# Kernel optimization log

Measured on AMD Instinct MI355X. Metric: run time of the kernel, lower is better.

Reference implementation:

```python
import jax, jax.numpy as jnp
import numpy as np

N, E, IN, H, C = 50000, 800000, 128, 256, 2
EPS = 1e-5


def setup_inputs() -> dict:
    key = jax.random.key(0)
    ks = jax.random.split(key, 12)
    inp = {
        "x": jax.random.normal(ks[0], (N, IN), jnp.float32),
        "edge_index": jax.random.randint(ks[1], (2, E), 0, N, jnp.int32),
        "w_nei0": jax.random.normal(ks[2], (IN, H), jnp.float32) * 0.05,
        "w_root0": jax.random.normal(ks[3], (IN, H), jnp.float32) * 0.05,
        "b0": jnp.zeros((H,), jnp.float32),
        "w_nei": jax.random.normal(ks[4], (2, H, H), jnp.float32) * 0.05,
        "w_root": jax.random.normal(ks[5], (2, H, H), jnp.float32) * 0.05,
        "b": jnp.zeros((2, H), jnp.float32),
        "bn_gamma": jnp.ones((3, H), jnp.float32),
        "bn_beta": jnp.zeros((3, H), jnp.float32),
        "bn_mean": jax.random.normal(ks[6], (3, H), jnp.float32) * 0.05,
        "bn_var": jnp.ones((3, H), jnp.float32),
        "w1": jax.random.normal(ks[7], (H, H // 2), jnp.float32) * 0.05,
        "b1": jnp.zeros((H // 2,), jnp.float32),
        "w2": jax.random.normal(ks[8], (H // 2, C), jnp.float32) * 0.05,
        "b2": jnp.zeros((C,), jnp.float32),
    }
    return inp


def _mean_aggregate(h, src, dst, inv_deg):
    # gather source-node features, scatter-sum to destinations, divide by degree
    agg = jax.ops.segment_sum(h[src], dst, num_segments=N)  # (N, d)
    return agg * inv_deg[:, None]


def _forward(x, edge_index, w_nei0, w_root0, b0, w_nei, w_root, b,
             bn_gamma, bn_beta, bn_mean, bn_var, w1, b1, w2, b2):
    src, dst = edge_index[0], edge_index[1]
    deg = jax.ops.segment_sum(jnp.ones((E,), x.dtype), dst, num_segments=N)
    inv_deg = 1.0 / jnp.maximum(deg, 1.0)

    h = x
    wn_list = [w_nei0, w_nei[0], w_nei[1]]
    wr_list = [w_root0, w_root[0], w_root[1]]
    bias_list = [b0, b[0], b[1]]
    for i in range(3):
        mean_nb = _mean_aggregate(h, src, dst, inv_deg)          # (N, d_in)
        h = mean_nb @ wn_list[i] + bias_list[i] + h @ wr_list[i]  # SAGEConv
        # BatchNorm1d (eval: running stats) + ReLU; dropout is identity in eval
        h = (h - bn_mean[i]) * jax.lax.rsqrt(bn_var[i] + EPS) * bn_gamma[i] + bn_beta[i]
        h = jax.nn.relu(h)

    h = jax.nn.relu(h @ w1 + b1)
    logits = h @ w2 + b2
    return jax.nn.log_softmax(logits, axis=1)


def reference(x, edge_index, w_nei0, w_root0, b0, w_nei, w_root, b,
              bn_gamma, bn_beta, bn_mean, bn_var, w1, b1, w2, b2):
    return _forward(x, edge_index, w_nei0, w_root0, b0, w_nei, w_root, b,
                    bn_gamma, bn_beta, bn_mean, bn_var, w1, b1, w2, b2)
```

## Files before the change

### kernel.cpp

```cpp
#include <hip/hip_runtime.h>
#include <hip/hip_fp16.h>

#define N_NODES 50000
#define N_EDGES 800000
#define DIM_IN 128
#define DIM_H 256

typedef _Float16 f16;
typedef _Float16 half8 __attribute__((ext_vector_type(8)));
typedef _Float16 f16x4 __attribute__((ext_vector_type(4)));
typedef _Float16 f16x2 __attribute__((ext_vector_type(2)));
typedef float f32x4 __attribute__((ext_vector_type(4)));
typedef unsigned int u32;

__device__ __forceinline__ void gload_lds16(const void* g, void* l) {
    __builtin_amdgcn_global_load_lds(
        (const __attribute__((address_space(1))) u32*)g,
        (__attribute__((address_space(3))) u32*)l,
        16, 0, 0);
}


__global__ void k_deg(const int* __restrict__ dst, int* __restrict__ deg) {
    int i = blockIdx.x * 256 + threadIdx.x;
    if (i < N_EDGES) atomicAdd(&deg[dst[i]], 1);
}

__global__ void k_scan1(const int* __restrict__ deg, int* __restrict__ row_start,
                        int* __restrict__ partials) {
    __shared__ int sm[256];
    int t = threadIdx.x;
    int i = blockIdx.x * 256 + t;
    int v = (i < N_NODES) ? deg[i] : 0;
    sm[t] = v;
    __syncthreads();
    for (int ofs = 1; ofs < 256; ofs <<= 1) {
        int add = (t >= ofs) ? sm[t - ofs] : 0;
        __syncthreads();
        sm[t] += add;
        __syncthreads();
    }
    if (i < N_NODES) row_start[i] = sm[t] - v;
    if (t == 255) partials[blockIdx.x] = sm[255];
}

__global__ void k_scan2(const int* __restrict__ partials, int* __restrict__ pscan, int nblk) {
    __shared__ int sm[256];
    int t = threadIdx.x;
    int v = (t < nblk) ? partials[t] : 0;
    sm[t] = v;
    __syncthreads();
    for (int ofs = 1; ofs < 256; ofs <<= 1) {
        int add = (t >= ofs) ? sm[t - ofs] : 0;
        __syncthreads();
        sm[t] += add;
        __syncthreads();
    }
    pscan[t] = sm[t] - v;
}

__global__ void k_scan3(const int* __restrict__ deg, int* __restrict__ row_start,
                        const int* __restrict__ pscan, float* __restrict__ inv_deg) {
    int i = blockIdx.x * 256 + threadIdx.x;
    if (i < N_NODES) {
        row_start[i] += pscan[blockIdx.x];
        int d = deg[i];
        inv_deg[i] = 1.0f / (float)(d > 1 ? d : 1);
        if (i == 0) row_start[N_NODES] = N_EDGES;
    }
}

__global__ void k_fill(const int* __restrict__ src, const int* __restrict__ dst,
                       const int* __restrict__ row_start, int* __restrict__ cursor,
                       int* __restrict__ csr) {
    int i = blockIdx.x * 256 + threadIdx.x;
    if (i < N_EDGES) {
        int d = dst[i];
        int p = atomicAdd(&cursor[d], 1);
        csr[row_start[d] + p] = src[i];
    }
}


__global__ void k_cvt_x(const float* __restrict__ x, f16* __restrict__ o) {
    int i = blockIdx.x * 256 + threadIdx.x;
    if (i < N_NODES * DIM_IN / 4) {
        float4 v = ((const float4*)x)[i];
        f16x4 h = {(f16)v.x, (f16)v.y, (f16)v.z, (f16)v.w};
        *(f16x4*)(o + (size_t)i * 4) = h;
    }
}

__global__ void k_tcvt(const float* __restrict__ W, f16* __restrict__ Wt, int K, int NN) {
    int t = blockIdx.x * 256 + threadIdx.x;
    if (t < K * NN) {
        int n = t / K, k = t - n * K;
        Wt[t] = (f16)W[(size_t)k * NN + n];
    }
}

__global__ void k_st(const float* __restrict__ b0, const float* __restrict__ bvec,
                     const float* __restrict__ gamma, const float* __restrict__ beta,
                     const float* __restrict__ mean, const float* __restrict__ var,
                     const float* __restrict__ b1, float* __restrict__ st) {
    int c = threadIdx.x;
    for (int layer = 0; layer < 3; layer++) {
        float bias = (layer == 0) ? b0[c] : bvec[(layer - 1) * DIM_H + c];
        float g = gamma[layer * DIM_H + c];
        float be = beta[layer * DIM_H + c];
        float mu = mean[layer * DIM_H + c];
        float va = var[layer * DIM_H + c];
        float s = g * rsqrtf(va + 1e-5f);
        st[layer * 512 + c] = s;
        st[layer * 512 + 256 + c] = (bias - mu) * s + be;
    }
    st[3 * 512 + c] = 1.0f;
    st[3 * 512 + 256 + c] = (c < 128) ? b1[c] : 0.0f;
}


template <int D>
__global__ void k_agg(const f16* __restrict__ h, const int* __restrict__ row_start,
                      const int* __restrict__ csr, const float* __restrict__ inv_deg,
                      f16* __restrict__ agg) {
    constexpr int V = D / 64;
    typedef _Float16 fvec __attribute__((ext_vector_type(V)));
    int wid = threadIdx.x >> 6;
    int lane = threadIdx.x & 63;
    int v = blockIdx.x * 4 + wid;
    if (v >= N_NODES) return;
    int e0 = row_start[v], e1 = row_start[v + 1];
    float acc[V];
#pragma unroll
    for (int j = 0; j < V; j++) acc[j] = 0.0f;

    const int li = lane & 15;
    for (int e = e0; e < e1; e += 16) {
        int ee = e + li;
        int idx = csr[ee < e1 ? ee : e1 - 1];
        int rem = e1 - e;
        fvec hv[16];
#pragma unroll
        for (int j = 0; j < 16; j++) {
            int s = __shfl(idx, j);
            hv[j] = *(const fvec*)(h + (size_t)s * D + lane * V);
        }
#pragma unroll
        for (int j = 0; j < 16; j++) {
            if (j < rem) {
#pragma unroll
                for (int q = 0; q < V; q++) acc[q] += (float)hv[j][q];
            }
        }
    }

    float sc = inv_deg[v];
    fvec o;
#pragma unroll
    for (int j = 0; j < V; j++) o[j] = (f16)(acc[j] * sc);
    *(fvec*)(agg + (size_t)v * D + lane * V) = o;
}


__global__ __launch_bounds__(256) void k_gemm(
    const f16* __restrict__ A1, int lda1, const f16* __restrict__ B1, int k1,
    const f16* __restrict__ A2, int lda2, const f16* __restrict__ B2, int k2,
    const float* __restrict__ sc, const float* __restrict__ sh,
    f16* __restrict__ out, int ldo, int M) {
    __shared__ f16 aT[2][64 * 32];
    __shared__ f16 bT[2][256 * 32];
    const int tid = threadIdx.x;
    const int lane = tid & 63;
    const int wid = tid >> 6;
    const int m0 = blockIdx.x * 64;
    f32x4 acc[4][4] = {};

    const int srow = tid >> 2;
    const int schunk = (tid & 3) ^ ((tid >> 3) & 3);
    const int ktot = k1 + k2;

    auto stage = [&](int buf, int kk) {
        const f16 *Ap, *Bp;
        int lda, ldb, kloc;
        if (kk < k1) { Ap = A1; Bp = B1; lda = lda1; ldb = k1; kloc = kk; }
        else         { Ap = A2; Bp = B2; lda = lda2; ldb = k2; kloc = kk - k1; }
        int gm = m0 + srow;
        gm = gm < M ? gm : M - 1;
        gload_lds16(Ap + (size_t)gm * lda + kloc + schunk * 8,
                    (char*)&aT[buf][0] + tid * 16);
#pragma unroll
        for (int hh = 0; hh < 4; hh++) {
            gload_lds16(Bp + (size_t)(hh * 64 + srow) * ldb + kloc + schunk * 8,
                        (char*)&bT[buf][0] + hh * 4096 + tid * 16);
        }
    };

    auto compute = [&](int buf) {
        half8 af[4], bf[4];
#pragma unroll
        for (int mi = 0; mi < 4; mi++) {
            int row = mi * 16 + (lane & 15);
            int ch = (lane >> 4) ^ ((row >> 1) & 3);
            af[mi] = *(const half8*)((const char*)&aT[buf][0] + row * 64 + ch * 16);
        }
#pragma unroll
        for (int ni = 0; ni < 4; ni++) {
            int row = wid * 64 + ni * 16 + (lane & 15);
            int ch = (lane >> 4) ^ ((row >> 1) & 3);
            bf[ni] = *(const half8*)((const char*)&bT[buf][0] + row * 64 + ch * 16);
        }
#pragma unroll
        for (int mi = 0; mi < 4; mi++)
#pragma unroll
            for (int ni = 0; ni < 4; ni++)
                acc[mi][ni] = __builtin_amdgcn_mfma_f32_16x16x32_f16(af[mi], bf[ni],
                                                                     acc[mi][ni], 0, 0, 0);
    };

    stage(0, 0);
    __syncthreads();
    int cur = 0;
    for (int kk = 32; kk < ktot; kk += 32) {
        stage(cur ^ 1, kk);
        compute(cur);
        __syncthreads();
        cur ^= 1;
    }
    compute(cur);

#pragma unroll
    for (int mi = 0; mi < 4; mi++) {
#pragma unroll
        for (int ni = 0; ni < 4; ni++) {
            int gcol = wid * 64 + ni * 16 + (lane & 15);
            float s = sc[gcol], t = sh[gcol];
#pragma unroll
            for (int r = 0; r < 4; r++) {
                int grow = m0 + mi * 16 + (lane >> 4) * 4 + r;
                if (grow < M) {
                    float val = fmaxf(acc[mi][ni][r] * s + t, 0.0f);
                    out[(size_t)grow * ldo + gcol] = (f16)val;
                }
            }
        }
    }
}


__global__ __launch_bounds__(256) void k_gemm_head(
    const f16* __restrict__ A1, int k1, const f16* __restrict__ B1,
    const float* __restrict__ sh,
    const float* __restrict__ w2, const float* __restrict__ b2,
    float* __restrict__ out, int M) {
    __shared__ f16 aT[2][128 * 32];
    __shared__ f16 bT[2][128 * 32];
    __shared__ float smred[128][2][2];
    const int tid = threadIdx.x;
    const int lane = tid & 63;
    const int wid = tid >> 6;
    const int wm = wid >> 1, wn = wid & 1;
    const int m0 = blockIdx.x * 128;
    f32x4 acc[4][4] = {};

    const int srow = tid >> 2;
    const int schunk = (tid & 3) ^ ((tid >> 3) & 3);

    auto stage = [&](int buf, int kk) {
#pragma unroll
        for (int hh = 0; hh < 2; hh++) {
            int r = hh * 64 + srow;
            int gm = m0 + r;
            gm = gm < M ? gm : M - 1;
            gload_lds16(A1 + (size_t)gm * k1 + kk + schunk * 8,
                        (char*)&aT[buf][0] + hh * 4096 + tid * 16);
            gload_lds16(B1 + (size_t)r * k1 + kk + schunk * 8,
                        (char*)&bT[buf][0] + hh * 4096 + tid * 16);
        }
    };

    auto compute = [&](int buf) {
        half8 af[4], bf[4];
#pragma unroll
        for (int mi = 0; mi < 4; mi++) {
            int row = wm * 64 + mi * 16 + (lane & 15);
            int ch = (lane >> 4) ^ ((row >> 1) & 3);
            af[mi] = *(const half8*)((const char*)&aT[buf][0] + row * 64 + ch * 16);
        }
#pragma unroll
        for (int ni = 0; ni < 4; ni++) {
            int row = wn * 64 + ni * 16 + (lane & 15);
            int ch = (lane >> 4) ^ ((row >> 1) & 3);
            bf[ni] = *(const half8*)((const char*)&bT[buf][0] + row * 64 + ch * 16);
        }
#pragma unroll
        for (int mi = 0; mi < 4; mi++)
#pragma unroll
            for (int ni = 0; ni < 4; ni++)
                acc[mi][ni] = __builtin_amdgcn_mfma_f32_16x16x32_f16(af[mi], bf[ni],
                                                                     acc[mi][ni], 0, 0, 0);
    };

    stage(0, 0);
    __syncthreads();
    int cur = 0;
    for (int kk = 32; kk < k1; kk += 32) {
        stage(cur ^ 1, kk);
        compute(cur);
        __syncthreads();
        cur ^= 1;
    }
    compute(cur);

    float w2c[4][2], shc[4];
#pragma unroll
    for (int ni = 0; ni < 4; ni++) {
        int c = wn * 64 + ni * 16 + (lane & 15);
        w2c[ni][0] = w2[c * 2];
        w2c[ni][1] = w2[c * 2 + 1];
        shc[ni] = sh[c];
    }
#pragma unroll
    for (int mi = 0; mi < 4; mi++) {
#pragma unroll
        for (int r = 0; r < 4; r++) {
            float p0 = 0.0f, p1 = 0.0f;
#pragma unroll
            for (int ni = 0; ni < 4; ni++) {
                float val = fmaxf(acc[mi][ni][r] + shc[ni], 0.0f);
                p0 += val * w2c[ni][0];
                p1 += val * w2c[ni][1];
            }
#pragma unroll
            for (int o = 1; o < 16; o <<= 1) {
                p0 += __shfl_xor(p0, o);
                p1 += __shfl_xor(p1, o);
            }
            if ((lane & 15) == 0) {
                int lrow = wm * 64 + mi * 16 + (lane >> 4) * 4 + r;
                smred[lrow][wn][0] = p0;
                smred[lrow][wn][1] = p1;
            }
        }
    }
    __syncthreads();
    if (tid < 128) {
        int grow = m0 + tid;
        if (grow < M) {
            float l0 = smred[tid][0][0] + smred[tid][1][0] + b2[0];
            float l1 = smred[tid][0][1] + smred[tid][1][1] + b2[1];
            float m = fmaxf(l0, l1);
            float lse = m + logf(expf(l0 - m) + expf(l1 - m));
            out[(size_t)grow * 2] = l0 - lse;
            out[(size_t)grow * 2 + 1] = l1 - lse;
        }
    }
}


extern "C" void kernel_launch(void* const* d_in, const int* in_sizes, int n_in,
                              void* d_out, int out_size, void* d_ws, size_t ws_size,
                              hipStream_t stream) {
    const float* x     = (const float*)d_in[0];
    const int*   ei    = (const int*)d_in[1];
    const float* wn0   = (const float*)d_in[2];
    const float* wr0   = (const float*)d_in[3];
    const float* b0    = (const float*)d_in[4];
    const float* wn12  = (const float*)d_in[5];
    const float* wr12  = (const float*)d_in[6];
    const float* bvec  = (const float*)d_in[7];
    const float* gamma = (const float*)d_in[8];
    const float* beta  = (const float*)d_in[9];
    const float* mean  = (const float*)d_in[10];
    const float* var   = (const float*)d_in[11];
    const float* w1    = (const float*)d_in[12];
    const float* b1    = (const float*)d_in[13];
    const float* w2    = (const float*)d_in[14];
    const float* b2    = (const float*)d_in[15];
    const int* srcv = ei;
    const int* dstv = ei + N_EDGES;

    char* p = (char*)d_ws;
    auto alloc = [&](size_t bytes) {
        char* r = p;
        p += (bytes + 255) & ~(size_t)255;
        return r;
    };
    int*   deg       = (int*)alloc((size_t)N_NODES * 4);
    int*   row_start = (int*)alloc((size_t)(N_NODES + 1) * 4);
    int*   cursor    = (int*)alloc((size_t)N_NODES * 4);
    float* inv_deg   = (float*)alloc((size_t)N_NODES * 4);
    int*   partials  = (int*)alloc(256 * 4);
    int*   pscan     = (int*)alloc(256 * 4);
    int*   csr       = (int*)alloc((size_t)N_EDGES * 4);
    f16*   Wn0t      = (f16*)alloc(128 * 256 * 2);
    f16*   Wr0t      = (f16*)alloc(128 * 256 * 2);
    f16*   Wn1t      = (f16*)alloc(256 * 256 * 2);
    f16*   Wr1t      = (f16*)alloc(256 * 256 * 2);
    f16*   Wn2t      = (f16*)alloc(256 * 256 * 2);
    f16*   Wr2t      = (f16*)alloc(256 * 256 * 2);
    f16*   W1t       = (f16*)alloc(256 * 128 * 2);
    float* st        = (float*)alloc(4 * 512 * 4);
    f16*   hA        = (f16*)alloc((size_t)N_NODES * 256 * 2);
    f16*   hB        = (f16*)alloc((size_t)N_NODES * 256 * 2);
    f16*   agg       = (f16*)alloc((size_t)N_NODES * 256 * 2);

    hipMemsetAsync(deg, 0, (size_t)N_NODES * 4, stream);
    hipMemsetAsync(cursor, 0, (size_t)N_NODES * 4, stream);

    const int EB = (N_EDGES + 255) / 256;
    const int NBLK = (N_NODES + 255) / 256;
    k_deg<<<EB, 256, 0, stream>>>(dstv, deg);
    k_scan1<<<NBLK, 256, 0, stream>>>(deg, row_start, partials);
    k_scan2<<<1, 256, 0, stream>>>(partials, pscan, NBLK);
    k_scan3<<<NBLK, 256, 0, stream>>>(deg, row_start, pscan, inv_deg);
    k_fill<<<EB, 256, 0, stream>>>(srcv, dstv, row_start, cursor, csr);

    k_cvt_x<<<(N_NODES * DIM_IN / 4 + 255) / 256, 256, 0, stream>>>(x, hA);
    k_tcvt<<<128, 256, 0, stream>>>(wn0, Wn0t, 128, 256);
    k_tcvt<<<128, 256, 0, stream>>>(wr0, Wr0t, 128, 256);
    k_tcvt<<<256, 256, 0, stream>>>(wn12, Wn1t, 256, 256);
    k_tcvt<<<256, 256, 0, stream>>>(wn12 + 65536, Wn2t, 256, 256);
    k_tcvt<<<256, 256, 0, stream>>>(wr12, Wr1t, 256, 256);
    k_tcvt<<<256, 256, 0, stream>>>(wr12 + 65536, Wr2t, 256, 256);
    k_tcvt<<<128, 256, 0, stream>>>(w1, W1t, 256, 128);
    k_st<<<1, 256, 0, stream>>>(b0, bvec, gamma, beta, mean, var, b1, st);

    const int AB = (N_NODES + 3) / 4;
    const int GB = (N_NODES + 63) / 64;

    k_agg<128><<<AB, 256, 0, stream>>>(hA, row_start, csr, inv_deg, agg);
    k_gemm<<<GB, 256, 0, stream>>>(agg, 128, Wn0t, 128, hA, 128, Wr0t, 128,
                                   st + 0, st + 256, hB, 256, N_NODES);
    k_agg<256><<<AB, 256, 0, stream>>>(hB, row_start, csr, inv_deg, agg);
    k_gemm<<<GB, 256, 0, stream>>>(agg, 256, Wn1t, 256, hB, 256, Wr1t, 256,
                                   st + 512, st + 768, hA, 256, N_NODES);
    k_agg<256><<<AB, 256, 0, stream>>>(hA, row_start, csr, inv_deg, agg);
    k_gemm<<<GB, 256, 0, stream>>>(agg, 256, Wn2t, 256, hA, 256, Wr2t, 256,
                                   st + 1024, st + 1280, hB, 256, N_NODES);
    k_gemm_head<<<(N_NODES + 127) / 128, 256, 0, stream>>>(
        hB, 256, W1t, st + 1792, w2, b2, (float*)d_out, N_NODES);
}
```

Baseline: 369.7 us.

## Split neighbor aggregation into eight feature slices across blocks

```diff
diff --git a/kernel.cpp b/kernel.cpp
--- a/kernel.cpp
+++ b/kernel.cpp
@@ -120,45 +120,51 @@
 
 
 template <int D>
-__global__ void k_agg(const f16* __restrict__ h, const int* __restrict__ row_start,
-                      const int* __restrict__ csr, const float* __restrict__ inv_deg,
-                      f16* __restrict__ agg) {
-    constexpr int V = D / 64;
+__global__ void k_aggx(const f16* __restrict__ h, const int* __restrict__ row_start,
+                       const int* __restrict__ csr, const float* __restrict__ inv_deg,
+                       f16* __restrict__ agg, int nchunks) {
+    constexpr int SL = D / 8;
+    constexpr int V = SL / 4;
     typedef _Float16 fvec __attribute__((ext_vector_type(V)));
-    int wid = threadIdx.x >> 6;
-    int lane = threadIdx.x & 63;
-    int v = blockIdx.x * 4 + wid;
-    if (v >= N_NODES) return;
-    int e0 = row_start[v], e1 = row_start[v + 1];
-    float acc[V];
-#pragma unroll
-    for (int j = 0; j < V; j++) acc[j] = 0.0f;
-
-    const int li = lane & 15;
-    for (int e = e0; e < e1; e += 16) {
-        int ee = e + li;
-        int idx = csr[ee < e1 ? ee : e1 - 1];
-        int rem = e1 - e;
-        fvec hv[16];
-#pragma unroll
-        for (int j = 0; j < 16; j++) {
-            int s = __shfl(idx, j);
-            hv[j] = *(const fvec*)(h + (size_t)s * D + lane * V);
-        }
-#pragma unroll
-        for (int j = 0; j < 16; j++) {
-            if (j < rem) {
-#pragma unroll
-                for (int q = 0; q < V; q++) acc[q] += (float)hv[j][q];
+    const int s = blockIdx.x & 7;
+    const int c = blockIdx.x >> 3;
+    const int wid = threadIdx.x >> 6;
+    const int lane = threadIdx.x & 63;
+    const int sub = lane & 3;
+    const int eg = lane >> 2;
+    const int nb = (N_NODES + nchunks - 1) / nchunks;
+    const int vbeg = c * nb;
+    const int vend = (vbeg + nb < N_NODES) ? vbeg + nb : N_NODES;
+    const f16* hs = h + s * SL + sub * V;
+
+    for (int v = vbeg + wid; v < vend; v += 4) {
+        int e0 = row_start[v], e1 = row_start[v + 1];
+        float acc[V];
+#pragma unroll
+        for (int q = 0; q < V; q++) acc[q] = 0.0f;
+
+        for (int e = e0; e < e1; e += 16) {
+            int ee = e + eg;
+            int idx = csr[ee < e1 ? ee : e1 - 1];
+            fvec hv = *(const fvec*)(hs + (size_t)idx * D);
+            if (ee < e1) {
+#pragma unroll
+                for (int q = 0; q < V; q++) acc[q] += (float)hv[q];
             }
         }
-    }
-
-    float sc = inv_deg[v];
-    fvec o;
-#pragma unroll
-    for (int j = 0; j < V; j++) o[j] = (f16)(acc[j] * sc);
-    *(fvec*)(agg + (size_t)v * D + lane * V) = o;
+#pragma unroll
+        for (int m = 4; m <= 32; m <<= 1) {
+#pragma unroll
+            for (int q = 0; q < V; q++) acc[q] += __shfl_xor(acc[q], m);
+        }
+        if (lane < 4) {
+            float scv = inv_deg[v];
+            fvec o;
+#pragma unroll
+            for (int q = 0; q < V; q++) o[q] = (f16)(acc[q] * scv);
+            *(fvec*)(agg + (size_t)v * D + s * SL + lane * V) = o;
+        }
+    }
 }
 
 
@@ -425,16 +431,17 @@
     k_tcvt<<<128, 256, 0, stream>>>(w1, W1t, 256, 128);
     k_st<<<1, 256, 0, stream>>>(b0, bvec, gamma, beta, mean, var, b1, st);
 
-    const int AB = (N_NODES + 3) / 4;
+    const int NCHUNKS = 1024;
+    const int AGB = 8 * NCHUNKS;
     const int GB = (N_NODES + 63) / 64;
 
-    k_agg<128><<<AB, 256, 0, stream>>>(hA, row_start, csr, inv_deg, agg);
+    k_aggx<128><<<AGB, 256, 0, stream>>>(hA, row_start, csr, inv_deg, agg, NCHUNKS);
     k_gemm<<<GB, 256, 0, stream>>>(agg, 128, Wn0t, 128, hA, 128, Wr0t, 128,
                                    st + 0, st + 256, hB, 256, N_NODES);
-    k_agg<256><<<AB, 256, 0, stream>>>(hB, row_start, csr, inv_deg, agg);
+    k_aggx<256><<<AGB, 256, 0, stream>>>(hB, row_start, csr, inv_deg, agg, NCHUNKS);
     k_gemm<<<GB, 256, 0, stream>>>(agg, 256, Wn1t, 256, hB, 256, Wr1t, 256,
                                    st + 512, st + 768, hA, 256, N_NODES);
-    k_agg<256><<<AB, 256, 0, stream>>>(hA, row_start, csr, inv_deg, agg);
+    k_aggx<256><<<AGB, 256, 0, stream>>>(hA, row_start, csr, inv_deg, agg, NCHUNKS);
     k_gemm<<<GB, 256, 0, stream>>>(agg, 256, Wn2t, 256, hA, 256, Wr2t, 256,
                                    st + 1024, st + 1280, hB, 256, N_NODES);
     k_gemm_head<<<(N_NODES + 127) / 128, 256, 0, stream>>>(
```

Result: slower. 618.4 us (+67.3%).
